# Kernel optimization log

Hardware: AMD Instinct MI355X
Metric: run time of the kernel (lower is better)

## Reference

```python
import math
import jax, jax.numpy as jnp
import numpy as np

LEVELS = 4          # wavelet_levels
PRUNE = 0.05        # wavelet_packet_prune_ratio
EPS = 1e-6
SQRT2 = math.sqrt(2.0)


def _haar_split(c):
    n = c.shape[-1]
    if n % 2 != 0:
        c = jnp.concatenate([c, jnp.zeros(c.shape[:-1] + (1,), c.dtype)], axis=-1)
    even, odd = c[..., 0::2], c[..., 1::2]
    return (even + odd) / SQRT2, (even - odd) / SQRT2, n


def _haar_merge(low, high, orig):
    even = (low + high) / SQRT2
    odd = (low - high) / SQRT2
    out = jnp.stack([even, odd], axis=-1).reshape(*low.shape[:-1], low.shape[-1] * 2)
    return out[..., :orig]


def _coherence(c, gpu):
    unit = c / jnp.maximum(jnp.abs(c), EPS)
    return jnp.clip(jnp.abs(jnp.mean(unit * jnp.conj(gpu), axis=-1, keepdims=True)), 0.0, 1.0)


def _cost(c, gpu):
    # gauge-aware packet cost: Shannon entropy of energy distribution + (1 - coherence)
    if c.shape[-1] <= 1:
        return jnp.float32(0.0)
    e = jnp.square(jnp.abs(c))
    p = jnp.maximum(e / jnp.maximum(e.sum(-1, keepdims=True), EPS), EPS)
    ent = -(p * jnp.log(p)).sum(-1)
    coh = _coherence(c, gpu)[..., 0]
    return jax.lax.stop_gradient(jnp.mean(ent + (1.0 - coh)))


def _band_center(path):
    if not path:
        return 0.0
    idx = 0
    for b in path:
        idx = (idx << 1) | b
    return (idx + 0.5) / (2 ** len(path))


def _leaf_gain(c, path, depth, gpu, Wp, bp, Wo, bo, lfg, sigma, hfg, cutoff):
    mag = jnp.maximum(jnp.abs(c), EPS)
    phase = jnp.arctan2(c.imag, c.real) / math.pi
    nle = jnp.broadcast_to(
        jnp.log(jnp.maximum(jnp.mean(jnp.square(jnp.abs(c)), -1, keepdims=True), EPS)), mag.shape)
    dn = jnp.full(mag.shape, depth / max(1, LEVELS), mag.dtype)
    bcv = _band_center(path)
    bc = jnp.full(mag.shape, bcv, mag.dtype)
    coh = jnp.broadcast_to(_coherence(c, gpu), mag.shape)
    pos = jnp.broadcast_to(jnp.linspace(0.0, 1.0, c.shape[-1], dtype=mag.dtype), mag.shape)
    feats = jnp.stack([jnp.log(mag), phase, nle, dn, bc, coh, pos], axis=-1)  # [..., n, 7]
    gd = jax.nn.silu(feats @ Wp.T + bp) @ Wo.T + bo                            # [..., n, 2]
    dm = 0.25 * jnp.tanh(gd[..., 0])
    dp = 0.5 * math.pi * jnp.tanh(gd[..., 1])
    lbb = 1.0 + lfg * jnp.exp(-(bcv * bcv) / jnp.square(sigma))
    hbd = hfg + (1.0 - hfg) * jax.nn.sigmoid((cutoff - bcv) / sigma)
    gm = lbb * hbd * (1.0 + lfg * coh) * (hfg + (1.0 - hfg) * coh) * jnp.exp(dm)
    return jax.lax.complex(gm * jnp.cos(dp), gm * jnp.sin(dp))  # torch.polar


def _filter_leaf(c, path, depth, total_e, gpu, params):
    Wp, bp, Wo, bo, lfg, sigma, hfg, cutoff = params
    node_e = jax.lax.stop_gradient(jnp.square(jnp.abs(c)).sum())
    filtered = c * _leaf_gain(c, path, depth, gpu, Wp, bp, Wo, bo, lfg, sigma, hfg, cutoff)
    coh_v = jax.lax.stop_gradient(jnp.mean(_coherence(c, gpu)))
    # spectral subtraction
    fm = jnp.abs(filtered)
    nf = jnp.median(fm, axis=-1, keepdims=True)
    damping = hfg + (1.0 - hfg) * jax.nn.sigmoid((cutoff - _band_center(path)) / sigma)
    den = jax.nn.relu(fm - (1.0 - damping) * nf)
    filtered = den * (filtered / jnp.maximum(fm, EPS))
    # prune low-energy / low-coherence leaves
    prune = jnp.logical_or(node_e / total_e < PRUNE, coh_v < PRUNE)
    return jnp.where(prune, filtered * jnp.square(hfg), filtered)


def _apply_node(c, depth, path, total_e, gpu, params):
    cost = _cost(c, gpu)
    leaf = _filter_leaf(c, path, depth, total_e, gpu, params)
    if depth >= LEVELS or c.shape[-1] <= 1:
        return leaf, cost
    low, high, orig = _haar_split(c)
    lr, lc = _apply_node(low, depth + 1, path + (0,), total_e, gpu, params)
    hr, hc = _apply_node(high, depth + 1, path + (1,), total_e, gpu, params)
    merged = _haar_merge(lr, hr, orig)
    child_cost = lc + hc
    # best-basis selection (wavelet_packet_best_basis=True)
    out = jnp.where(child_cost < cost, merged, leaf)
    return out, jnp.minimum(child_cost, cost)


def setup_inputs() -> dict:
    key = jax.random.key(0)
    ks = jax.random.split(key, 3)
    B, R, N = 8, 64, 8192
    x = jax.random.normal(ks[0], (B, R, N), jnp.float32)
    Wp = jax.random.normal(ks[1], (12, 7), jnp.float32) * math.sqrt(2.0 / 19.0)  # xavier-ish
    bp = jnp.zeros((12,), jnp.float32)
    Wo = jax.random.normal(ks[2], (2, 12), jnp.float32) * 0.1
    bo = jnp.zeros((2,), jnp.float32)
    return {"x": x, "Wp": Wp, "bp": bp, "Wo": Wo, "bo": bo,
            "lfg": jnp.float32(0.5), "sigma": jnp.float32(0.3),
            "hfg": jnp.float32(0.7), "cutoff": jnp.float32(0.25)}


def reference(x, Wp, bp, Wo, bo, lfg, sigma, hfg, cutoff):
    n = x.shape[-1]
    spec = jnp.fft.fft(x)  # complex64 [B, R, N]
    # _fft_filter spectral gating
    r2 = jnp.square(jnp.fft.fftfreq(n).astype(x.dtype))
    lfb = 1.0 + lfg * jnp.exp(-r2 / jnp.square(sigma))
    radius = jnp.sqrt(r2 + 1e-12)
    gate = jax.nn.sigmoid((cutoff - radius) / jnp.maximum(sigma, 0.05))
    spec = spec * (lfb * (hfg + (1.0 - hfg) * gate))
    # global phase unit
    unit = spec / jnp.maximum(jnp.abs(spec), EPS)
    g = jnp.mean(unit, axis=-1, keepdims=True)
    gpu = g / jnp.maximum(jnp.abs(g), EPS)
    total_e = jax.lax.stop_gradient(jnp.square(jnp.abs(spec)).sum())
    params = (Wp, bp, Wo, bo, lfg, sigma, hfg, cutoff)
    out, _ = _apply_node(spec, 0, (), total_e, gpu, params)
    return jnp.fft.ifft(out).real
```

## Files before the change

kernel.cpp:

```cpp
#include <hip/hip_runtime.h>
#include <hip/hip_fp16.h>
#include <math.h>

#define NN      8192
#define LOGN    13
#define ROWS    512
#define NT      512
#define NNODES  31
#define EPSF    1e-6f
#define PRUNEF  0.05f
#define SQRT1_2F 0.70710678118654752f
#define PIF      3.14159265358979323f
#define INV_PIF  0.31830988618379067f
#define HALF_PIF 1.57079632679489662f

typedef unsigned int uint;

__device__ __forceinline__ float fast_rcp(float x){ return __builtin_amdgcn_rcpf(x); }
__device__ __forceinline__ float fast_rsq(float x){ return __builtin_amdgcn_rsqf(x); }

__device__ __forceinline__ float tanh_pade(float y){
    y = fminf(3.f, fmaxf(-3.f, y));
    float y2 = y * y;
    float num = y * fmaf(y2, 10.f, 105.f);
    float den = fmaf(y2, 45.f, fmaf(y2 * y2, 1.f, 105.f));
    return num * fast_rcp(den);
}
__device__ __forceinline__ float silu_pade(float h){
    float y = fminf(3.f, fmaxf(-3.f, 0.5f * h));
    float y2 = y * y;
    float num = y * fmaf(y2, 10.f, 105.f);
    float den = fmaf(y2, 45.f, fmaf(y2 * y2, 1.f, 105.f));
    return 0.5f * h * (1.f + num * fast_rcp(den));
}
__device__ __forceinline__ float exp_small(float z){
    return fmaf(z, fmaf(z, fmaf(z, fmaf(z, 0.041666667f, 0.16666667f), 0.5f), 1.f), 1.f);
}
__device__ __forceinline__ float sin_halfpi(float t){
    float t2 = t * t;
    return t * fmaf(t2, fmaf(t2, fmaf(t2, -4.6817541e-3f, 7.96926262e-2f), -6.45964097e-1f), 1.57079632f);
}
__device__ __forceinline__ float cos_halfpi(float t){
    float t2 = t * t;
    return fmaf(t2, fmaf(t2, fmaf(t2, fmaf(t2, 9.1937e-4f, -2.08634807e-2f), 2.53669508e-1f), -1.23370055f), 1.f);
}

__device__ __forceinline__ float fast_atan2f(float y, float x) {
    float ay = fabsf(y), ax = fabsf(x);
    float mx = fmaxf(ax, ay), mn = fminf(ax, ay);
    float a = (mx > 0.f) ? (mn * fast_rcp(mx)) : 0.f;
    bool big = a > 0.4142135679f;
    float t = big ? ((a - 1.f) * fast_rcp(a + 1.f)) : a;
    float z2 = t * t;
    float p = fmaf(8.05374449538e-2f, z2, -1.38776856032e-1f);
    p = fmaf(p, z2, 1.99777106478e-1f);
    p = fmaf(p, z2, -3.33329491539e-1f);
    float r = fmaf(p * z2, t, t);
    if (big) r += 0.78539816339744831f;
    if (ay > ax) r = 1.57079632679489662f - r;
    if (x < 0.f) r = 3.14159265358979323f - r;
    return copysignf(r, y);
}

__device__ __forceinline__ float2 cmul(float2 a, float2 b){
    return make_float2(a.x*b.x - a.y*b.y, a.x*b.y + a.y*b.x);
}
__device__ __forceinline__ float2 cadd(float2 a, float2 b){ return make_float2(a.x+b.x, a.y+b.y); }
__device__ __forceinline__ float2 csub(float2 a, float2 b){ return make_float2(a.x-b.x, a.y-b.y); }

__device__ __forceinline__ uint pack_h2(float2 v){
    __half2 h = __floats2half2_rn(v.x, v.y);
    return __builtin_bit_cast(uint, h);
}
__device__ __forceinline__ float2 unpack_h2(uint u){
    __half2 h = __builtin_bit_cast(__half2, u);
    return make_float2(__low2float(h), __high2float(h));
}

__device__ __forceinline__ void wave_red8(float* a) {
    #pragma unroll
    for (int m = 32; m >= 1; m >>= 1) {
        #pragma unroll
        for (int q = 0; q < 8; ++q) a[q] += __shfl_xor(a[q], m);
    }
}

#define C8C 0.92387953251f
#define S8C 0.38268343236f
#define C4C 0.70710678119f

template<int HH, int LG>
__device__ __forceinline__ void fwd_r4_stage(float2* sh, int tid) {
    int j = tid & (HH - 1);
    float ang = (-PIF / (2.0f * (float)HH)) * (float)j;
    float s = __sinf(ang), co = __cosf(ang);
    float2 t1 = make_float2(co, s);
    float2 t2 = make_float2(co * co - s * s, 2.f * co * s);
    int g = tid & 127;
    int i = ((g >> LG) << (LG + 2)) | (g & (HH - 1));
    #pragma unroll
    for (int c = 0; c < 4; ++c) {
        int lb = (tid + (c << 9)) >> 7;
        int p = (lb << 9) + i;
        float2 a = sh[p], b = sh[p + HH], cc = sh[p + 2*HH], d = sh[p + 3*HH];
        float2 a1 = cadd(a, cc);
        float2 c1 = cmul(csub(a, cc), t1);
        float2 b1 = cadd(b, d);
        float2 u  = cmul(csub(b, d), t1);
        float2 d1 = make_float2(u.y, -u.x);
        sh[p]        = cadd(a1, b1);
        sh[p + HH]   = cmul(csub(a1, b1), t2);
        sh[p + 2*HH] = cadd(c1, d1);
        sh[p + 3*HH] = cmul(csub(c1, d1), t2);
    }
    __syncthreads();
}

template<int H, int LG>
__device__ __forceinline__ void inv_r4_stage(float2* sh, int tid) {
    int jj = tid & (H - 1);
    float ang = (PIF / (2.0f * (float)H)) * (float)jj;
    float s2 = __sinf(ang), c2 = __cosf(ang);
    float2 t2 = make_float2(c2, s2);
    float2 t1 = make_float2(c2 * c2 - s2 * s2, 2.f * c2 * s2);
    int g = tid & 127;
    int i = ((g >> LG) << (LG + 2)) | (g & (H - 1));
    #pragma unroll
    for (int c = 0; c < 4; ++c) {
        int lb = (tid + (c << 9)) >> 7;
        int p0 = (lb << 9) + i;
        float2 a = sh[p0], b = sh[p0 + H], cc = sh[p0 + 2*H], d = sh[p0 + 3*H];
        float2 tb = cmul(t1, b);
        float2 ap = cadd(a, tb), bp2 = csub(a, tb);
        float2 td = cmul(t1, d);
        float2 cp = cadd(cc, td), dp2 = csub(cc, td);
        float2 tc = cmul(t2, cp);
        float2 u  = cmul(t2, dp2);
        float2 iB = make_float2(-u.y, u.x);
        sh[p0]       = cadd(ap, tc);
        sh[p0 + H]   = cadd(bp2, iB);
        sh[p0 + 2*H] = csub(ap, tc);
        sh[p0 + 3*H] = csub(bp2, iB);
    }
    __syncthreads();
}

__global__ __launch_bounds__(NT, 4) void k_pre(
    const float* __restrict__ x, uint* __restrict__ Lv16,
    float* __restrict__ Se, float* __restrict__ Coh, float* __restrict__ Ent,
    const float* lfg_p, const float* sig_p, const float* hfg_p, const float* cut_p)
{
    __shared__ float2 sh[NN];
    __shared__ float4 wred[8];
    __shared__ float nacc[30 * 4];
    int row = blockIdx.x, tid = threadIdx.x;
    float lfg = *lfg_p, sigma = *sig_p, hfg = *hfg_p, cutoff = *cut_p;

    const float* xr = x + ((size_t)row << LOGN);
    float2 v[16];
    #pragma unroll
    for (int t = 0; t < 16; ++t)
        v[t] = make_float2(xr[tid + (t << 9)], 0.f);

    {
        float a0 = -PIF * (1.0f / 4096.0f) * (float)tid;
        float2 w1 = make_float2(__cosf(a0), __sinf(a0));
        float2 w2 = cmul(w1, w1);
        float2 w4 = cmul(w2, w2);
        float2 w8 = cmul(w4, w4);
        const float2 K16[8] = {
            { 1.f, 0.f}, { C8C, -S8C}, { C4C, -C4C}, { S8C, -C8C},
            { 0.f,-1.f}, {-S8C, -C8C}, {-C4C, -C4C}, {-C8C, -S8C}};
        #pragma unroll
        for (int t = 0; t < 8; ++t) {
            float2 W = cmul(w1, K16[t]);
            float2 a = v[t], b = v[t + 8];
            v[t] = cadd(a, b);
            v[t + 8] = cmul(csub(a, b), W);
        }
        const float2 K8a[4] = {{1.f,0.f},{C4C,-C4C},{0.f,-1.f},{-C4C,-C4C}};
        #pragma unroll
        for (int t = 0; t < 16; ++t) if (!(t & 4)) {
            float2 W = cmul(w2, K8a[t & 3]);
            float2 a = v[t], b = v[t + 4];
            v[t] = cadd(a, b);
            v[t + 4] = cmul(csub(a, b), W);
        }
        #pragma unroll
        for (int t = 0; t < 16; ++t) if (!(t & 2)) {
            float2 W = (t & 1) ? make_float2(w4.y, -w4.x) : w4;
            float2 a = v[t], b = v[t + 2];
            v[t] = cadd(a, b);
            v[t + 2] = cmul(csub(a, b), W);
        }
        #pragma unroll
        for (int t = 0; t < 16; ++t) if (!(t & 1)) {
            float2 a = v[t], b = v[t + 1];
            v[t] = cadd(a, b);
            v[t + 1] = cmul(csub(a, b), w8);
        }
    }

    if (tid < 120) nacc[tid] = 0.f;

    #pragma unroll
    for (int t = 0; t < 16; ++t) sh[tid + (t << 9)] = v[t];
    __syncthreads();
    fwd_r4_stage<128, 7>(sh, tid);
    fwd_r4_stage<32, 5>(sh, tid);
    fwd_r4_stage<8, 3>(sh, tid);
    fwd_r4_stage<2, 1>(sh, tid);
    #pragma unroll
    for (int c = 0; c < 8; ++c) {
        int p = (tid + (c << 9)) << 1;
        float2 a = sh[p], b = sh[p + 1];
        sh[p] = cadd(a, b);
        sh[p + 1] = csub(a, b);
    }
    __syncthreads();

    float inv_gs = 1.f / fmaxf(sigma, 0.05f);
    float is2 = 1.f / (sigma * sigma);
    float se = 0.f, slg = 0.f, sux = 0.f, suy = 0.f;
    #pragma unroll
    for (int t = 0; t < 16; ++t) {
        int p = tid + (t << 9);
        int k = (int)(__brev((uint)p) >> 19);
        float fk = (k < NN / 2) ? (float)k : (float)(k - NN);
        float f = fk * (1.0f / (float)NN);
        float r2 = f * f;
        float lfb = 1.f + lfg * __expf(-r2 * is2);
        float radius = sqrtf(r2 + 1e-12f);
        float gate = fast_rcp(1.f + __expf(-(cutoff - radius) * inv_gs));
        float mult = lfb * (hfg + (1.f - hfg) * gate);
        float2 c = sh[p];
        c.x *= mult; c.y *= mult;
        v[t] = c;
        float e = fmaf(c.x, c.x, c.y * c.y);
        se += e;
        slg += e * __logf(fmaxf(e, 1e-30f));
        float inv = fminf(fast_rsq(e), 1e6f);
        sux += c.x * inv; suy += c.y * inv;
    }
    #pragma unroll
    for (int m = 32; m >= 1; m >>= 1) {
        se += __shfl_xor(se, m); slg += __shfl_xor(slg, m);
        sux += __shfl_xor(sux, m); suy += __shfl_xor(suy, m);
    }
    if ((tid & 63) == 0) wred[tid >> 6] = make_float4(se, slg, sux, suy);
    __syncthreads();
    if (tid == 0) {
        float4 r = wred[0];
        #pragma unroll
        for (int w = 1; w < 8; ++w) {
            r.x += wred[w].x; r.y += wred[w].y; r.z += wred[w].z; r.w += wred[w].w;
        }
        float gx = r.z / (float)NN, gy = r.w / (float)NN;
        float ga = sqrtf(gx * gx + gy * gy);
        float denom = fmaxf(r.x, EPSF);
        Se[row]  = r.x;
        Ent[row] = __logf(denom) - r.y / denom;
        Coh[row] = fminf(ga, 1.f);
    }

    #pragma unroll
    for (int DP = 0; DP < 4; ++DP) {
        int ST = 8 >> DP;
        #pragma unroll
        for (int t = 0; t < 16; ++t) {
            if ((t & ST) == 0) {
                float2 a = v[t], b = v[t + ST];
                v[t]      = make_float2((a.x + b.x) * SQRT1_2F, (a.y + b.y) * SQRT1_2F);
                v[t + ST] = make_float2((a.x - b.x) * SQRT1_2F, (a.y - b.y) * SQRT1_2F);
            }
        }
        int CNT = 16 >> (DP + 1);
        int NPAIR = 1 << DP;
        int G0 = (2 << DP) - 1;
        #pragma unroll
        for (int pr = 0; pr < NPAIR; ++pr) {
            float acc[8] = {0,0,0,0,0,0,0,0};
            #pragma unroll
            for (int s = 0; s < 16; ++s) {
                int k0 = s - (2 * pr) * CNT;
                if (k0 >= 0 && k0 < CNT) {
                    float2 w = v[s];
                    float e = fmaf(w.x, w.x, w.y * w.y);
                    acc[0] += e; acc[1] += e * __logf(fmaxf(e, 1e-30f));
                    float iv = fminf(fast_rsq(e), 1e6f);
                    acc[2] += w.x * iv; acc[3] += w.y * iv;
                }
                int k1 = s - (2 * pr + 1) * CNT;
                if (k1 >= 0 && k1 < CNT) {
                    float2 w = v[s];
                    float e = fmaf(w.x, w.x, w.y * w.y);
                    acc[4] += e; acc[5] += e * __logf(fmaxf(e, 1e-30f));
                    float iv = fminf(fast_rsq(e), 1e6f);
                    acc[6] += w.x * iv; acc[7] += w.y * iv;
                }
            }
            wave_red8(acc);
            if ((tid & 63) == 0) {
                int ga = G0 + 2 * pr, gb = ga + 1;
                atomicAdd(&nacc[(ga-1)*4+0], acc[0]); atomicAdd(&nacc[(ga-1)*4+1], acc[1]);
                atomicAdd(&nacc[(ga-1)*4+2], acc[2]); atomicAdd(&nacc[(ga-1)*4+3], acc[3]);
                atomicAdd(&nacc[(gb-1)*4+0], acc[4]); atomicAdd(&nacc[(gb-1)*4+1], acc[5]);
                atomicAdd(&nacc[(gb-1)*4+2], acc[6]); atomicAdd(&nacc[(gb-1)*4+3], acc[7]);
            }
        }
    }
    __syncthreads();
    if (tid < 30) {
        int g = tid + 1;
        float E = nacc[tid * 4 + 0], SL = nacc[tid * 4 + 1];
        float ZX = nacc[tid * 4 + 2], ZY = nacc[tid * 4 + 3];
        float denom = fmaxf(E, EPSF);
        float ent = __logf(denom) - SL / denom;
        int d = 31 - __clz(g + 1);
        float invn = 1.f / (float)(NN >> d);
        float zx = ZX * invn, zy = ZY * invn;
        float ch = fminf(sqrtf(zx * zx + zy * zy), 1.f);
        Se[g * ROWS + row] = E; Coh[g * ROWS + row] = ch; Ent[g * ROWS + row] = ent;
    }

    uint* lrow = Lv16 + ((size_t)row << LOGN);
    #pragma unroll
    for (int t = 0; t < 16; ++t)
        lrow[tid + (t << 9)] = pack_h2(v[t]);
}

__global__ __launch_bounds__(NT) void k_decide(
    const float* __restrict__ Se, const float* __restrict__ Coh, const float* __restrict__ Ent,
    int* __restrict__ fFg, int* __restrict__ fPg)
{
    __shared__ float dtmp[3 * NNODES];
    __shared__ int fF[NNODES], fP[NNODES];
    int tid = threadIdx.x;
    float* dcost = dtmp; float* dne = dtmp + NNODES; float* dcm = dtmp + 2 * NNODES;
    int wid = tid >> 6, lane = tid & 63;
    for (int gn = wid; gn < NNODES; gn += 8) {
        float a = 0.f, b = 0.f, cc = 0.f;
        #pragma unroll
        for (int rr = 0; rr < ROWS / 64; ++rr) {
            int r = lane + (rr << 6);
            float ch = Coh[gn * ROWS + r];
            a += Ent[gn * ROWS + r] + 1.f - ch;
            b += Se[gn * ROWS + r];
            cc += ch;
        }
        #pragma unroll
        for (int m = 32; m >= 1; m >>= 1) {
            a += __shfl_xor(a, m); b += __shfl_xor(b, m); cc += __shfl_xor(cc, m);
        }
        if (lane == 0) { dcost[gn] = a / (float)ROWS; dne[gn] = b; dcm[gn] = cc / (float)ROWS; }
    }
    __syncthreads();
    if (tid == 0) {
        float mc[NNODES]; int sel[NNODES]; int act[NNODES];
        for (int gn = NNODES - 1; gn >= 0; --gn) {
            if (gn >= 15) { mc[gn] = dcost[gn]; sel[gn] = 0; }
            else {
                float chc = mc[2 * gn + 1] + mc[2 * gn + 2];
                sel[gn] = (chc < dcost[gn]) ? 1 : 0;
                mc[gn] = fminf(chc, dcost[gn]);
            }
        }
        float total_e = dne[0];
        act[0] = 1;
        for (int gn = 1; gn < NNODES; ++gn) {
            int p = (gn - 1) >> 1;
            act[gn] = act[p] && sel[p];
        }
        for (int gn = 0; gn < NNODES; ++gn) {
            int isleaf = (gn >= 15);
            fF[gn] = (act[gn] && (isleaf || !sel[gn])) ? 1 : 0;
            fP[gn] = ((dne[gn] / total_e < PRUNEF) || (dcm[gn] < PRUNEF)) ? 1 : 0;
        }
    }
    __syncthreads();
    if (tid < NNODES) { fFg[tid] = fF[tid]; fPg[tid] = fP[tid]; }
}

__device__ __forceinline__ uint key_of(float2 v) {
    return __float_as_uint(fmaf(v.x, v.x, v.y * v.y));
}
__device__ __forceinline__ uint key_at(const float2* sh, int p) { return key_of(sh[p]); }

__device__ __forceinline__ uint2 hist_locate1024(
    const uint* hist, int tid, uint r, uint* wsum, uint* selres)
{
    uint l0 = hist[2 * tid], l1 = hist[2 * tid + 1];
    uint s = l0 + l1;
    uint sc = s;
    #pragma unroll
    for (int o = 1; o < 64; o <<= 1) {
        uint v = __shfl_up(sc, o);
        if ((tid & 63) >= o) sc += v;
    }
    int wid = tid >> 6;
    if ((tid & 63) == 63) wsum[wid] = sc;
    __syncthreads();
    uint wb = 0;
    #pragma unroll
    for (int w = 0; w < 8; ++w) if (w < wid) wb += wsum[w];
    uint c0 = wb + sc - s;
    if (r >= c0 && r < c0 + l0) { selres[0] = 2u * tid;      selres[1] = c0; }
    c0 += l0;
    if (r >= c0 && r < c0 + l1) { selres[0] = 2u * tid + 1u; selres[1] = c0; }
    __syncthreads();
    uint2 res = make_uint2(selres[0], selres[1]);
    __syncthreads();
    return res;
}

template<int EPT>
__device__ __forceinline__ float median_node(
    const float2* sh, int nd, int tid,
    uint* hist, uint* wsum, uint* selres)
{
    uint r1 = (uint)(nd / 2 - 1), r2 = (uint)(nd / 2);
    for (int k = tid; k < 1024; k += NT) hist[k] = 0u;
    __syncthreads();
    #pragma unroll
    for (int c = 0; c < EPT; ++c)
        atomicAdd(&hist[key_at(sh, tid + (c << 9)) >> 21], 1u);
    __syncthreads();
    uint2 A1 = hist_locate1024(hist, tid, r1, wsum, selres);
    uint2 A2 = hist_locate1024(hist, tid, r2, wsum, selres);
    uint va, vb;
    if (A1.x != A2.x) {
        if (tid == 0) { selres[0] = 0u; selres[1] = 0xFFFFFFFFu; }
        __syncthreads();
        #pragma unroll
        for (int c = 0; c < EPT; ++c) {
            uint k = key_at(sh, tid + (c << 9));
            uint b = k >> 21;
            if (b == A1.x) atomicMax(&selres[0], k);
            if (b == A2.x) atomicMin(&selres[1], k);
        }
        __syncthreads();
        va = selres[0]; vb = selres[1];
        __syncthreads();
    } else {
        uint p1 = A1.x;
        for (int k = tid; k < 1024; k += NT) hist[k] = 0u;
        __syncthreads();
        #pragma unroll
        for (int c = 0; c < EPT; ++c) {
            uint k = key_at(sh, tid + (c << 9));
            if ((k >> 21) == p1) atomicAdd(&hist[(k >> 11) & 1023u], 1u);
        }
        __syncthreads();
        uint2 B1 = hist_locate1024(hist, tid, r1 - A1.y, wsum, selres);
        uint2 B2 = hist_locate1024(hist, tid, r2 - A1.y, wsum, selres);
        if (B1.x != B2.x) {
            uint pA = (p1 << 10) | B1.x, pB = (p1 << 10) | B2.x;
            if (tid == 0) { selres[0] = 0u; selres[1] = 0xFFFFFFFFu; }
            __syncthreads();
            #pragma unroll
            for (int c = 0; c < EPT; ++c) {
                uint k = key_at(sh, tid + (c << 9));
                uint b = k >> 11;
                if (b == pA) atomicMax(&selres[0], k);
                if (b == pB) atomicMin(&selres[1], k);
            }
            __syncthreads();
            va = selres[0]; vb = selres[1];
            __syncthreads();
        } else {
            uint pfx = (p1 << 10) | B1.x;
            for (int k = tid; k < 1024; k += NT) hist[k] = 0u;
            __syncthreads();
            #pragma unroll
            for (int c = 0; c < EPT; ++c) {
                uint k = key_at(sh, tid + (c << 9));
                if ((k >> 11) == pfx) atomicAdd(&hist[(k >> 1) & 1023u], 1u);
            }
            __syncthreads();
            uint2 C1 = hist_locate1024(hist, tid, r1 - A1.y - B1.y, wsum, selres);
            uint2 C2 = hist_locate1024(hist, tid, r2 - A1.y - B1.y, wsum, selres);
            va = ((pfx << 10) | C1.x) << 1;
            vb = ((pfx << 10) | C2.x) << 1;
        }
    }
    return 0.5f * (sqrtf(__uint_as_float(va)) + sqrtf(__uint_as_float(vb)));
}

__device__ __forceinline__ float median_root_reg(
    const float2 (&v)[16], int tid, uint* hist, uint* wsum, uint* selres)
{
    const uint r1 = NN / 2 - 1, r2 = NN / 2;
    for (int k = tid; k < 1024; k += NT) hist[k] = 0u;
    __syncthreads();
    #pragma unroll
    for (int t = 0; t < 16; ++t)
        atomicAdd(&hist[key_of(v[t]) >> 21], 1u);
    __syncthreads();
    uint2 A1 = hist_locate1024(hist, tid, r1, wsum, selres);
    uint2 A2 = hist_locate1024(hist, tid, r2, wsum, selres);
    uint va, vb;
    if (A1.x != A2.x) {
        if (tid == 0) { selres[0] = 0u; selres[1] = 0xFFFFFFFFu; }
        __syncthreads();
        #pragma unroll
        for (int t = 0; t < 16; ++t) {
            uint k = key_of(v[t]);
            uint b = k >> 21;
            if (b == A1.x) atomicMax(&selres[0], k);
            if (b == A2.x) atomicMin(&selres[1], k);
        }
        __syncthreads();
        va = selres[0]; vb = selres[1];
        __syncthreads();
    } else {
        uint p1 = A1.x;
        for (int k = tid; k < 1024; k += NT) hist[k] = 0u;
        __syncthreads();
        #pragma unroll
        for (int t = 0; t < 16; ++t) {
            uint k = key_of(v[t]);
            if ((k >> 21) == p1) atomicAdd(&hist[(k >> 11) & 1023u], 1u);
        }
        __syncthreads();
        uint2 B1 = hist_locate1024(hist, tid, r1 - A1.y, wsum, selres);
        uint2 B2 = hist_locate1024(hist, tid, r2 - A1.y, wsum, selres);
        if (B1.x != B2.x) {
            uint pA = (p1 << 10) | B1.x, pB = (p1 << 10) | B2.x;
            if (tid == 0) { selres[0] = 0u; selres[1] = 0xFFFFFFFFu; }
            __syncthreads();
            #pragma unroll
            for (int t = 0; t < 16; ++t) {
                uint k = key_of(v[t]);
                uint b = k >> 11;
                if (b == pA) atomicMax(&selres[0], k);
                if (b == pB) atomicMin(&selres[1], k);
            }
            __syncthreads();
            va = selres[0]; vb = selres[1];
            __syncthreads();
        } else {
            uint pfx = (p1 << 10) | B1.x;
            for (int k = tid; k < 1024; k += NT) hist[k] = 0u;
            __syncthreads();
            #pragma unroll
            for (int t = 0; t < 16; ++t) {
                uint k = key_of(v[t]);
                if ((k >> 11) == pfx) atomicAdd(&hist[(k >> 1) & 1023u], 1u);
            }
            __syncthreads();
            uint2 C1 = hist_locate1024(hist, tid, r1 - A1.y - B1.y, wsum, selres);
            uint2 C2 = hist_locate1024(hist, tid, r2 - A1.y - B1.y, wsum, selres);
            va = ((pfx << 10) | C1.x) << 1;
            vb = ((pfx << 10) | C2.x) << 1;
        }
    }
    return 0.5f * (sqrtf(__uint_as_float(va)) + sqrtf(__uint_as_float(vb)));
}

struct NodeConst {
    float hbd, gbase, hb[12], bo0, bo1;
};
__device__ __forceinline__ NodeConst node_consts(
    int D, int nodes, int n, int g, int ND, int row,
    const float* __restrict__ Wp, const float* __restrict__ bp,
    const float* __restrict__ Wo, const float* __restrict__ bo,
    const float* __restrict__ Se, const float* __restrict__ Coh,
    float lfg, float sigma, float hfg, float cutoff)
{
    NodeConst nc;
    float bcv = (D == 0) ? 0.f : ((float)n + 0.5f) / (float)nodes;
    float coh = Coh[g * ROWS + row];
    float sev = Se[g * ROWS + row];
    float nle = __logf(fmaxf(sev * (1.f / (float)ND), EPSF));
    float dnv = (float)D * 0.25f;
    float lbb = 1.f + lfg * __expf(-(bcv * bcv) / (sigma * sigma));
    nc.hbd = hfg + (1.f - hfg) * fast_rcp(1.f + __expf(-(cutoff - bcv) / sigma));
    nc.gbase = lbb * nc.hbd * (1.f + lfg * coh) * (hfg + (1.f - hfg) * coh);
    #pragma unroll
    for (int j = 0; j < 12; ++j)
        nc.hb[j] = bp[j] + nle * Wp[j*7+2] + dnv * Wp[j*7+3] + bcv * Wp[j*7+4] + coh * Wp[j*7+5];
    nc.bo0 = bo[0]; nc.bo1 = bo[1];
    return nc;
}

__device__ __forceinline__ float2 mlp_apply(
    float2 cv, int o, int D, float invnm1, const NodeConst& nc,
    const float* __restrict__ Wp, const float* __restrict__ Wo)
{
    float m2 = fmaf(cv.x, cv.x, cv.y * cv.y);
    float f0 = 0.5f * __logf(fmaxf(m2, 1e-12f));
    float f1 = fast_atan2f(cv.y, cv.x) * INV_PIF;
    int itrue = (int)(__brev((uint)o) >> (19 + D));
    float f6 = (float)itrue * invnm1;
    float acc0 = nc.bo0, acc1 = nc.bo1;
    #pragma unroll
    for (int j = 0; j < 12; ++j) {
        float h = fmaf(f0, Wp[j*7], fmaf(f1, Wp[j*7+1], fmaf(f6, Wp[j*7+6], nc.hb[j])));
        float s = silu_pade(h);
        acc0 = fmaf(s, Wo[j], acc0);
        acc1 = fmaf(s, Wo[12 + j], acc1);
    }
    float gm = nc.gbase * exp_small(0.25f * tanh_pade(acc0));
    float tp = tanh_pade(acc1);
    float spv = sin_halfpi(tp), cpv = cos_halfpi(tp);
    return make_float2(gm * (cv.x * cpv - cv.y * spv),
                       gm * (cv.x * spv + cv.y * cpv));
}

template<int D>
__device__ __forceinline__ void filter_node_sh(
    float2 (&v)[16], int n, int tid, float2* sh,
    const float* __restrict__ Wp, const float* __restrict__ bp,
    const float* __restrict__ Wo, const float* __restrict__ bo,
    const float* __restrict__ Se, const float* __restrict__ Coh,
    const int* __restrict__ fPg, int row,
    uint* hist, uint* wsum, uint* selres,
    float lfg, float sigma, float hfg, float cutoff)
{
    constexpr int CNT = 16 >> D;
    constexpr int ND  = NN >> D;
    constexpr int EPT = ND >> 9;
    int g = (1 << D) - 1 + n;

    #pragma unroll
    for (int t = 0; t < 16; ++t) {
        int k = t - n * CNT;
        if ((unsigned)k < (unsigned)CNT) sh[tid + (k << 9)] = v[t];
    }
    __syncthreads();

    NodeConst nc = node_consts(D, 1 << D, n, g, ND, row, Wp, bp, Wo, bo, Se, Coh,
                               lfg, sigma, hfg, cutoff);
    float invnm1 = 1.f / (float)(ND - 1);

    #pragma unroll
    for (int c = 0; c < EPT; ++c) {
        int o = tid + (c << 9);
        sh[o] = mlp_apply(sh[o], o, D, invnm1, nc, Wp, Wo);
    }
    __syncthreads();

    float nf = median_node<EPT>(sh, ND, tid, hist, wsum, selres);
    float thr = (1.f - nc.hbd) * nf;
    float pf = fPg[g] ? (hfg * hfg) : 1.f;

    #pragma unroll
    for (int c = 0; c < EPT; ++c) {
        int o = tid + (c << 9);
        float2 w = sh[o];
        float fm = sqrtf(fmaf(w.x, w.x, w.y * w.y));
        float den = fmaxf(fm - thr, 0.f);
        float s = den * fast_rcp(fmaxf(fm, EPSF)) * pf;
        sh[o] = make_float2(w.x * s, w.y * s);
    }
    __syncthreads();

    #pragma unroll
    for (int t = 0; t < 16; ++t) {
        int k = t - n * CNT;
        if ((unsigned)k < (unsigned)CNT) v[t] = sh[tid + (k << 9)];
    }
    __syncthreads();
}

__device__ __forceinline__ void filter_root_reg(
    float2 (&v)[16], int tid,
    const float* __restrict__ Wp, const float* __restrict__ bp,
    const float* __restrict__ Wo, const float* __restrict__ bo,
    const float* __restrict__ Se, const float* __restrict__ Coh,
    const int* __restrict__ fPg, int row,
    uint* hist, uint* wsum, uint* selres,
    float lfg, float sigma, float hfg, float cutoff)
{
    NodeConst nc = node_consts(0, 1, 0, 0, NN, row, Wp, bp, Wo, bo, Se, Coh,
                               lfg, sigma, hfg, cutoff);
    float invnm1 = 1.f / (float)(NN - 1);

    #pragma unroll
    for (int t = 0; t < 16; ++t) {
        int o = tid + (t << 9);
        v[t] = mlp_apply(v[t], o, 0, invnm1, nc, Wp, Wo);
    }

    float nf = median_root_reg(v, tid, hist, wsum, selres);
    float thr = (1.f - nc.hbd) * nf;
    float pf = fPg[0] ? (hfg * hfg) : 1.f;

    #pragma unroll
    for (int t = 0; t < 16; ++t) {
        float2 w = v[t];
        float fm = sqrtf(fmaf(w.x, w.x, w.y * w.y));
        float den = fmaxf(fm - thr, 0.f);
        float s = den * fast_rcp(fmaxf(fm, EPSF)) * pf;
        v[t] = make_float2(w.x * s, w.y * s);
    }
}

template<int DT>
__device__ __forceinline__ void merge_reg(float2 (&v)[16]){
    #pragma unroll
    for (int t = 0; t < 16; ++t) {
        if ((t & DT) == 0) {
            float2 lo = v[t], hi = v[t + DT];
            v[t]      = make_float2((lo.x + hi.x) * SQRT1_2F, (lo.y + hi.y) * SQRT1_2F);
            v[t + DT] = make_float2((lo.x - hi.x) * SQRT1_2F, (lo.y - hi.y) * SQRT1_2F);
        }
    }
}

__global__ __launch_bounds__(NT, 4) void k_rest(
    const uint* __restrict__ Lv16,
    const float* __restrict__ Se, const float* __restrict__ Coh,
    const int* __restrict__ fFg, const int* __restrict__ fPg,
    float* __restrict__ out,
    const float* __restrict__ Wp, const float* __restrict__ bp,
    const float* __restrict__ Wo, const float* __restrict__ bo,
    const float* lfg_p, const float* sig_p, const float* hfg_p, const float* cut_p)
{
    __shared__ float2 sh[NN];
    __shared__ __align__(16) uint hist[1024];
    __shared__ uint wsum[8];
    __shared__ uint selres[2];

    int row = blockIdx.x, tid = threadIdx.x;
    float lfg = *lfg_p, sigma = *sig_p, hfg = *hfg_p, cutoff = *cut_p;

    const uint* lr = Lv16 + ((size_t)row << LOGN);
    uint raw[16];
    #pragma unroll
    for (int t = 0; t < 16; ++t) raw[t] = lr[tid + (t << 9)];

    float2 v[16];
    #pragma unroll
    for (int t = 0; t < 16; ++t) v[t] = unpack_h2(raw[t]);

    for (int n = 0; n < 16; ++n)
        if (fFg[15 + n])
            filter_node_sh<4>(v, n, tid, sh, Wp, bp, Wo, bo, Se, Coh, fPg, row, hist, wsum, selres, lfg, sigma, hfg, cutoff);
    merge_reg<1>(v);
    for (int n = 0; n < 8; ++n)
        if (fFg[7 + n])
            filter_node_sh<3>(v, n, tid, sh, Wp, bp, Wo, bo, Se, Coh, fPg, row, hist, wsum, selres, lfg, sigma, hfg, cutoff);
    merge_reg<2>(v);
    for (int n = 0; n < 4; ++n)
        if (fFg[3 + n])
            filter_node_sh<2>(v, n, tid, sh, Wp, bp, Wo, bo, Se, Coh, fPg, row, hist, wsum, selres, lfg, sigma, hfg, cutoff);
    merge_reg<4>(v);
    for (int n = 0; n < 2; ++n)
        if (fFg[1 + n])
            filter_node_sh<1>(v, n, tid, sh, Wp, bp, Wo, bo, Se, Coh, fPg, row, hist, wsum, selres, lfg, sigma, hfg, cutoff);
    merge_reg<8>(v);
    if (fFg[0])
        filter_root_reg(v, tid, Wp, bp, Wo, bo, Se, Coh, fPg, row, hist, wsum, selres, lfg, sigma, hfg, cutoff);

    #pragma unroll
    for (int t = 0; t < 16; ++t) sh[tid + (t << 9)] = v[t];
    __syncthreads();

    inv_r4_stage<1, 0>(sh, tid);
    inv_r4_stage<4, 2>(sh, tid);
    inv_r4_stage<16, 4>(sh, tid);
    inv_r4_stage<64, 6>(sh, tid);
    {
        int jj = tid & 255;
        float ang = (PIF / 256.0f) * (float)jj;
        float2 W = make_float2(__cosf(ang), __sinf(ang));
        #pragma unroll
        for (int c = 0; c < 8; ++c) {
            int q = tid + (c << 9);
            int lb = q >> 8;
            int p = (lb << 9) + jj;
            float2 a = sh[p], b = sh[p + 256];
            float2 tb = cmul(W, b);
            sh[p] = cadd(a, tb);
            sh[p + 256] = csub(a, tb);
        }
        __syncthreads();
    }

    #pragma unroll
    for (int t = 0; t < 16; ++t) v[t] = sh[tid + (t << 9)];
    {
        float a0 = PIF * (1.0f / 4096.0f) * (float)tid;
        float2 w1 = make_float2(__cosf(a0), __sinf(a0));
        float2 w2 = cmul(w1, w1);
        float2 w4 = cmul(w2, w2);
        float2 w8 = cmul(w4, w4);
        #pragma unroll
        for (int t = 0; t < 16; ++t) if (!(t & 1)) {
            float2 tb = cmul(w8, v[t + 1]);
            float2 a = v[t];
            v[t] = cadd(a, tb);
            v[t + 1] = csub(a, tb);
        }
        #pragma unroll
        for (int t = 0; t < 16; ++t) if (!(t & 2)) {
            float2 W = (t & 1) ? make_float2(-w4.y, w4.x) : w4;
            float2 tb = cmul(W, v[t + 2]);
            float2 a = v[t];
            v[t] = cadd(a, tb);
            v[t + 2] = csub(a, tb);
        }
        const float2 K8p[4] = {{1.f,0.f},{C4C,C4C},{0.f,1.f},{-C4C,C4C}};
        #pragma unroll
        for (int t = 0; t < 16; ++t) if (!(t & 4)) {
            float2 W = cmul(w2, K8p[t & 3]);
            float2 tb = cmul(W, v[t + 4]);
            float2 a = v[t];
            v[t] = cadd(a, tb);
            v[t + 4] = csub(a, tb);
        }
        const float2 K16p[8] = {
            { 1.f, 0.f}, { C8C, S8C}, { C4C, C4C}, { S8C, C8C},
            { 0.f, 1.f}, {-S8C, C8C}, {-C4C, C4C}, {-C8C, S8C}};
        #pragma unroll
        for (int t = 0; t < 8; ++t) {
            float2 W = cmul(w1, K16p[t]);
            float2 tb = cmul(W, v[t + 8]);
            float2 a = v[t];
            v[t] = cadd(a, tb);
            v[t + 8] = csub(a, tb);
        }
    }

    float* orow = out + ((size_t)row << LOGN);
    #pragma unroll
    for (int t = 0; t < 16; ++t)
        orow[tid + (t << 9)] = v[t].x * (1.0f / (float)NN);
}

extern "C" void kernel_launch(void* const* d_in, const int* in_sizes, int n_in,
                              void* d_out, int out_size, void* d_ws, size_t ws_size,
                              hipStream_t stream) {
    const float* x   = (const float*)d_in[0];
    const float* Wp  = (const float*)d_in[1];
    const float* bp  = (const float*)d_in[2];
    const float* Wo  = (const float*)d_in[3];
    const float* bo  = (const float*)d_in[4];
    const float* lfg = (const float*)d_in[5];
    const float* sig = (const float*)d_in[6];
    const float* hfg = (const float*)d_in[7];
    const float* cut = (const float*)d_in[8];
    float* out = (float*)d_out;

    size_t LVB = (size_t)ROWS * NN * sizeof(uint);
    char* ws = (char*)d_ws;
    uint*   Lv16 = (uint*)ws;
    float*  Se   = (float*)(ws + LVB);
    float*  Coh  = Se  + (size_t)NNODES * ROWS;
    float*  Ent  = Coh + (size_t)NNODES * ROWS;
    int*    fFg  = (int*)(Ent + (size_t)NNODES * ROWS);
    int*    fPg  = fFg + NNODES;
    size_t need = (size_t)((char*)(fPg + NNODES) - ws);
    if (ws_size < need) return;

    dim3 b(NT);
    k_pre   <<<dim3(ROWS), b, 0, stream>>>(x, Lv16, Se, Coh, Ent, lfg, sig, hfg, cut);
    k_decide<<<dim3(1),    b, 0, stream>>>(Se, Coh, Ent, fFg, fPg);
    k_rest  <<<dim3(ROWS), b, 0, stream>>>(Lv16, Se, Coh, fFg, fPg, out, Wp, bp, Wo, bo, lfg, sig, hfg, cut);
}
```

Baseline: 131.3 us.

## Double threads per row to 1024 and restructure FFT and wavelet stages for 8 elements per thread

Raises the block size from 512 to 1024 threads, so each thread holds 8 complex values instead of 16. The in-register radix-16 FFT prologue and epilogue become radix-8, and the shared-memory radix-4 stages are re-indexed. The last wavelet split and merge level now goes through shared memory, and the per-node median and filter code is made generic over node size. The intent is more wave-level parallelism and lower register pressure per thread, at the cost of extra shared-memory round-trips, more __syncthreads barriers and more atomics per block.

```diff
diff --git a/kernel.cpp b/kernel.cpp
--- a/kernel.cpp
+++ b/kernel.cpp
@@ -5,14 +5,13 @@
 #define NN      8192
 #define LOGN    13
 #define ROWS    512
-#define NT      512
+#define NT      1024
 #define NNODES  31
 #define EPSF    1e-6f
 #define PRUNEF  0.05f
 #define SQRT1_2F 0.70710678118654752f
 #define PIF      3.14159265358979323f
 #define INV_PIF  0.31830988618379067f
-#define HALF_PIF 1.57079632679489662f
 
 typedef unsigned int uint;
 
@@ -85,8 +84,6 @@
     }
 }
 
-#define C8C 0.92387953251f
-#define S8C 0.38268343236f
 #define C4C 0.70710678119f
 
 template<int HH, int LG>
@@ -96,12 +93,10 @@
     float s = __sinf(ang), co = __cosf(ang);
     float2 t1 = make_float2(co, s);
     float2 t2 = make_float2(co * co - s * s, 2.f * co * s);
-    int g = tid & 127;
-    int i = ((g >> LG) << (LG + 2)) | (g & (HH - 1));
-    #pragma unroll
-    for (int c = 0; c < 4; ++c) {
-        int lb = (tid + (c << 9)) >> 7;
-        int p = (lb << 9) + i;
+    #pragma unroll
+    for (int c = 0; c < 2; ++c) {
+        int q = tid + (c << 10);
+        int p = ((q >> LG) << (LG + 2)) | j;
         float2 a = sh[p], b = sh[p + HH], cc = sh[p + 2*HH], d = sh[p + 3*HH];
         float2 a1 = cadd(a, cc);
         float2 c1 = cmul(csub(a, cc), t1);
@@ -123,12 +118,10 @@
     float s2 = __sinf(ang), c2 = __cosf(ang);
     float2 t2 = make_float2(c2, s2);
     float2 t1 = make_float2(c2 * c2 - s2 * s2, 2.f * c2 * s2);
-    int g = tid & 127;
-    int i = ((g >> LG) << (LG + 2)) | (g & (H - 1));
-    #pragma unroll
-    for (int c = 0; c < 4; ++c) {
-        int lb = (tid + (c << 9)) >> 7;
-        int p0 = (lb << 9) + i;
+    #pragma unroll
+    for (int c = 0; c < 2; ++c) {
+        int q = tid + (c << 10);
+        int p0 = ((q >> LG) << (LG + 2)) | jj;
         float2 a = sh[p0], b = sh[p0 + H], cc = sh[p0 + 2*H], d = sh[p0 + 3*H];
         float2 tb = cmul(t1, b);
         float2 ap = cadd(a, tb), bp2 = csub(a, tb);
@@ -145,86 +138,82 @@
     __syncthreads();
 }
 
-__global__ __launch_bounds__(NT, 4) void k_pre(
+__global__ __launch_bounds__(NT, 8) void k_pre(
     const float* __restrict__ x, uint* __restrict__ Lv16,
     float* __restrict__ Se, float* __restrict__ Coh, float* __restrict__ Ent,
     const float* lfg_p, const float* sig_p, const float* hfg_p, const float* cut_p)
 {
     __shared__ float2 sh[NN];
-    __shared__ float4 wred[8];
+    __shared__ float4 wred[16];
     __shared__ float nacc[30 * 4];
     int row = blockIdx.x, tid = threadIdx.x;
     float lfg = *lfg_p, sigma = *sig_p, hfg = *hfg_p, cutoff = *cut_p;
 
     const float* xr = x + ((size_t)row << LOGN);
-    float2 v[16];
-    #pragma unroll
-    for (int t = 0; t < 16; ++t)
-        v[t] = make_float2(xr[tid + (t << 9)], 0.f);
+    float2 v[8];
+    #pragma unroll
+    for (int t = 0; t < 8; ++t)
+        v[t] = make_float2(xr[tid + (t << 10)], 0.f);
 
     {
         float a0 = -PIF * (1.0f / 4096.0f) * (float)tid;
         float2 w1 = make_float2(__cosf(a0), __sinf(a0));
         float2 w2 = cmul(w1, w1);
         float2 w4 = cmul(w2, w2);
-        float2 w8 = cmul(w4, w4);
-        const float2 K16[8] = {
-            { 1.f, 0.f}, { C8C, -S8C}, { C4C, -C4C}, { S8C, -C8C},
-            { 0.f,-1.f}, {-S8C, -C8C}, {-C4C, -C4C}, {-C8C, -S8C}};
-        #pragma unroll
-        for (int t = 0; t < 8; ++t) {
-            float2 W = cmul(w1, K16[t]);
-            float2 a = v[t], b = v[t + 8];
-            v[t] = cadd(a, b);
-            v[t + 8] = cmul(csub(a, b), W);
-        }
-        const float2 K8a[4] = {{1.f,0.f},{C4C,-C4C},{0.f,-1.f},{-C4C,-C4C}};
-        #pragma unroll
-        for (int t = 0; t < 16; ++t) if (!(t & 4)) {
-            float2 W = cmul(w2, K8a[t & 3]);
+        const float2 K4m[4] = {{1.f,0.f},{C4C,-C4C},{0.f,-1.f},{-C4C,-C4C}};
+        #pragma unroll
+        for (int t = 0; t < 4; ++t) {
+            float2 W = cmul(w1, K4m[t]);
             float2 a = v[t], b = v[t + 4];
             v[t] = cadd(a, b);
             v[t + 4] = cmul(csub(a, b), W);
         }
         #pragma unroll
-        for (int t = 0; t < 16; ++t) if (!(t & 2)) {
-            float2 W = (t & 1) ? make_float2(w4.y, -w4.x) : w4;
+        for (int t = 0; t < 8; ++t) if (!(t & 2)) {
+            float2 W = (t & 1) ? make_float2(w2.y, -w2.x) : w2;
             float2 a = v[t], b = v[t + 2];
             v[t] = cadd(a, b);
             v[t + 2] = cmul(csub(a, b), W);
         }
         #pragma unroll
-        for (int t = 0; t < 16; ++t) if (!(t & 1)) {
+        for (int t = 0; t < 8; ++t) if (!(t & 1)) {
             float2 a = v[t], b = v[t + 1];
             v[t] = cadd(a, b);
-            v[t + 1] = cmul(csub(a, b), w8);
-        }
+            v[t + 1] = cmul(csub(a, b), w4);
+        }
+    }
+
+    #pragma unroll
+    for (int t = 0; t < 8; ++t) sh[tid + (t << 10)] = v[t];
+    __syncthreads();
+    fwd_r4_stage<256, 8>(sh, tid);
+    fwd_r4_stage<64, 6>(sh, tid);
+    fwd_r4_stage<16, 4>(sh, tid);
+    fwd_r4_stage<4, 2>(sh, tid);
+    {
+        #pragma unroll
+        for (int c = 0; c < 2; ++c) {
+            int p = (tid + (c << 10)) << 2;
+            float2 a = sh[p], b = sh[p+1], cc = sh[p+2], d = sh[p+3];
+            float2 a1 = cadd(a, cc), c1 = csub(a, cc);
+            float2 b1 = cadd(b, d);
+            float2 u  = csub(b, d);
+            float2 d1 = make_float2(u.y, -u.x);
+            sh[p]   = cadd(a1, b1);
+            sh[p+1] = csub(a1, b1);
+            sh[p+2] = cadd(c1, d1);
+            sh[p+3] = csub(c1, d1);
+        }
+        __syncthreads();
     }
 
     if (tid < 120) nacc[tid] = 0.f;
-
-    #pragma unroll
-    for (int t = 0; t < 16; ++t) sh[tid + (t << 9)] = v[t];
-    __syncthreads();
-    fwd_r4_stage<128, 7>(sh, tid);
-    fwd_r4_stage<32, 5>(sh, tid);
-    fwd_r4_stage<8, 3>(sh, tid);
-    fwd_r4_stage<2, 1>(sh, tid);
-    #pragma unroll
-    for (int c = 0; c < 8; ++c) {
-        int p = (tid + (c << 9)) << 1;
-        float2 a = sh[p], b = sh[p + 1];
-        sh[p] = cadd(a, b);
-        sh[p + 1] = csub(a, b);
-    }
-    __syncthreads();
-
     float inv_gs = 1.f / fmaxf(sigma, 0.05f);
     float is2 = 1.f / (sigma * sigma);
     float se = 0.f, slg = 0.f, sux = 0.f, suy = 0.f;
     #pragma unroll
-    for (int t = 0; t < 16; ++t) {
-        int p = tid + (t << 9);
+    for (int t = 0; t < 8; ++t) {
+        int p = tid + (t << 10);
         int k = (int)(__brev((uint)p) >> 19);
         float fk = (k < NN / 2) ? (float)k : (float)(k - NN);
         float f = fk * (1.0f / (float)NN);
@@ -252,7 +241,7 @@
     if (tid == 0) {
         float4 r = wred[0];
         #pragma unroll
-        for (int w = 1; w < 8; ++w) {
+        for (int w = 1; w < 16; ++w) {
             r.x += wred[w].x; r.y += wred[w].y; r.z += wred[w].z; r.w += wred[w].w;
         }
         float gx = r.z / (float)NN, gy = r.w / (float)NN;
@@ -263,50 +252,129 @@
         Coh[row] = fminf(ga, 1.f);
     }
 
-    #pragma unroll
-    for (int DP = 0; DP < 4; ++DP) {
-        int ST = 8 >> DP;
-        #pragma unroll
-        for (int t = 0; t < 16; ++t) {
-            if ((t & ST) == 0) {
-                float2 a = v[t], b = v[t + ST];
-                v[t]      = make_float2((a.x + b.x) * SQRT1_2F, (a.y + b.y) * SQRT1_2F);
-                v[t + ST] = make_float2((a.x - b.x) * SQRT1_2F, (a.y - b.y) * SQRT1_2F);
-            }
-        }
-        int CNT = 16 >> (DP + 1);
-        int NPAIR = 1 << DP;
-        int G0 = (2 << DP) - 1;
-        #pragma unroll
-        for (int pr = 0; pr < NPAIR; ++pr) {
+    {
+        #pragma unroll
+        for (int t = 0; t < 4; ++t) {
+            float2 a = v[t], b = v[t + 4];
+            v[t]     = make_float2((a.x + b.x) * SQRT1_2F, (a.y + b.y) * SQRT1_2F);
+            v[t + 4] = make_float2((a.x - b.x) * SQRT1_2F, (a.y - b.y) * SQRT1_2F);
+        }
+        float acc[8] = {0,0,0,0,0,0,0,0};
+        #pragma unroll
+        for (int s = 0; s < 4; ++s) {
+            float2 w = v[s];
+            float e = fmaf(w.x, w.x, w.y * w.y);
+            acc[0] += e; acc[1] += e * __logf(fmaxf(e, 1e-30f));
+            float iv = fminf(fast_rsq(e), 1e6f);
+            acc[2] += w.x * iv; acc[3] += w.y * iv;
+            float2 h = v[s + 4];
+            float e2 = fmaf(h.x, h.x, h.y * h.y);
+            acc[4] += e2; acc[5] += e2 * __logf(fmaxf(e2, 1e-30f));
+            float iv2 = fminf(fast_rsq(e2), 1e6f);
+            acc[6] += h.x * iv2; acc[7] += h.y * iv2;
+        }
+        wave_red8(acc);
+        if ((tid & 63) == 0) {
+            atomicAdd(&nacc[0], acc[0]); atomicAdd(&nacc[1], acc[1]);
+            atomicAdd(&nacc[2], acc[2]); atomicAdd(&nacc[3], acc[3]);
+            atomicAdd(&nacc[4], acc[4]); atomicAdd(&nacc[5], acc[5]);
+            atomicAdd(&nacc[6], acc[6]); atomicAdd(&nacc[7], acc[7]);
+        }
+    }
+    {
+        #pragma unroll
+        for (int t = 0; t < 8; ++t) if (!(t & 2)) {
+            float2 a = v[t], b = v[t + 2];
+            v[t]     = make_float2((a.x + b.x) * SQRT1_2F, (a.y + b.y) * SQRT1_2F);
+            v[t + 2] = make_float2((a.x - b.x) * SQRT1_2F, (a.y - b.y) * SQRT1_2F);
+        }
+        #pragma unroll
+        for (int pr = 0; pr < 2; ++pr) {
             float acc[8] = {0,0,0,0,0,0,0,0};
             #pragma unroll
-            for (int s = 0; s < 16; ++s) {
-                int k0 = s - (2 * pr) * CNT;
-                if (k0 >= 0 && k0 < CNT) {
-                    float2 w = v[s];
-                    float e = fmaf(w.x, w.x, w.y * w.y);
-                    acc[0] += e; acc[1] += e * __logf(fmaxf(e, 1e-30f));
-                    float iv = fminf(fast_rsq(e), 1e6f);
-                    acc[2] += w.x * iv; acc[3] += w.y * iv;
-                }
-                int k1 = s - (2 * pr + 1) * CNT;
-                if (k1 >= 0 && k1 < CNT) {
-                    float2 w = v[s];
-                    float e = fmaf(w.x, w.x, w.y * w.y);
-                    acc[4] += e; acc[5] += e * __logf(fmaxf(e, 1e-30f));
-                    float iv = fminf(fast_rsq(e), 1e6f);
-                    acc[6] += w.x * iv; acc[7] += w.y * iv;
-                }
+            for (int s = 0; s < 2; ++s) {
+                float2 w = v[4 * pr + s];
+                float e = fmaf(w.x, w.x, w.y * w.y);
+                acc[0] += e; acc[1] += e * __logf(fmaxf(e, 1e-30f));
+                float iv = fminf(fast_rsq(e), 1e6f);
+                acc[2] += w.x * iv; acc[3] += w.y * iv;
+                float2 h = v[4 * pr + 2 + s];
+                float e2 = fmaf(h.x, h.x, h.y * h.y);
+                acc[4] += e2; acc[5] += e2 * __logf(fmaxf(e2, 1e-30f));
+                float iv2 = fminf(fast_rsq(e2), 1e6f);
+                acc[6] += h.x * iv2; acc[7] += h.y * iv2;
             }
             wave_red8(acc);
             if ((tid & 63) == 0) {
-                int ga = G0 + 2 * pr, gb = ga + 1;
+                int ga = 3 + 2 * pr, gb = ga + 1;
                 atomicAdd(&nacc[(ga-1)*4+0], acc[0]); atomicAdd(&nacc[(ga-1)*4+1], acc[1]);
                 atomicAdd(&nacc[(ga-1)*4+2], acc[2]); atomicAdd(&nacc[(ga-1)*4+3], acc[3]);
                 atomicAdd(&nacc[(gb-1)*4+0], acc[4]); atomicAdd(&nacc[(gb-1)*4+1], acc[5]);
                 atomicAdd(&nacc[(gb-1)*4+2], acc[6]); atomicAdd(&nacc[(gb-1)*4+3], acc[7]);
             }
+        }
+    }
+    {
+        #pragma unroll
+        for (int t = 0; t < 8; ++t) if (!(t & 1)) {
+            float2 a = v[t], b = v[t + 1];
+            v[t]     = make_float2((a.x + b.x) * SQRT1_2F, (a.y + b.y) * SQRT1_2F);
+            v[t + 1] = make_float2((a.x - b.x) * SQRT1_2F, (a.y - b.y) * SQRT1_2F);
+        }
+        #pragma unroll
+        for (int pr = 0; pr < 4; ++pr) {
+            float acc[8] = {0,0,0,0,0,0,0,0};
+            {
+                float2 w = v[2 * pr];
+                float e = fmaf(w.x, w.x, w.y * w.y);
+                acc[0] = e; acc[1] = e * __logf(fmaxf(e, 1e-30f));
+                float iv = fminf(fast_rsq(e), 1e6f);
+                acc[2] = w.x * iv; acc[3] = w.y * iv;
+                float2 h = v[2 * pr + 1];
+                float e2 = fmaf(h.x, h.x, h.y * h.y);
+                acc[4] = e2; acc[5] = e2 * __logf(fmaxf(e2, 1e-30f));
+                float iv2 = fminf(fast_rsq(e2), 1e6f);
+                acc[6] = h.x * iv2; acc[7] = h.y * iv2;
+            }
+            wave_red8(acc);
+            if ((tid & 63) == 0) {
+                int ga = 7 + 2 * pr, gb = ga + 1;
+                atomicAdd(&nacc[(ga-1)*4+0], acc[0]); atomicAdd(&nacc[(ga-1)*4+1], acc[1]);
+                atomicAdd(&nacc[(ga-1)*4+2], acc[2]); atomicAdd(&nacc[(ga-1)*4+3], acc[3]);
+                atomicAdd(&nacc[(gb-1)*4+0], acc[4]); atomicAdd(&nacc[(gb-1)*4+1], acc[5]);
+                atomicAdd(&nacc[(gb-1)*4+2], acc[6]); atomicAdd(&nacc[(gb-1)*4+3], acc[7]);
+            }
+        }
+    }
+
+    #pragma unroll
+    for (int t = 0; t < 8; ++t) sh[tid + (t << 10)] = v[t];
+    __syncthreads();
+    #pragma unroll
+    for (int t = 0; t < 4; ++t) {
+        int q = tid + (t << 10);
+        int p = ((q >> 9) << 10) | (q & 511);
+        float2 a = sh[p], b = sh[p + 512];
+        float2 lo = make_float2((a.x + b.x) * SQRT1_2F, (a.y + b.y) * SQRT1_2F);
+        float2 hi = make_float2((a.x - b.x) * SQRT1_2F, (a.y - b.y) * SQRT1_2F);
+        sh[p] = lo; sh[p + 512] = hi;
+        float acc[8];
+        float e = fmaf(lo.x, lo.x, lo.y * lo.y);
+        acc[0] = e; acc[1] = e * __logf(fmaxf(e, 1e-30f));
+        float iv = fminf(fast_rsq(e), 1e6f);
+        acc[2] = lo.x * iv; acc[3] = lo.y * iv;
+        float e2 = fmaf(hi.x, hi.x, hi.y * hi.y);
+        acc[4] = e2; acc[5] = e2 * __logf(fmaxf(e2, 1e-30f));
+        float iv2 = fminf(fast_rsq(e2), 1e6f);
+        acc[6] = hi.x * iv2; acc[7] = hi.y * iv2;
+        wave_red8(acc);
+        if ((tid & 63) == 0) {
+            int ca = (q >> 9) << 1;
+            int ia = (14 + ca) * 4;
+            atomicAdd(&nacc[ia+0], acc[0]); atomicAdd(&nacc[ia+1], acc[1]);
+            atomicAdd(&nacc[ia+2], acc[2]); atomicAdd(&nacc[ia+3], acc[3]);
+            atomicAdd(&nacc[ia+4], acc[4]); atomicAdd(&nacc[ia+5], acc[5]);
+            atomicAdd(&nacc[ia+6], acc[6]); atomicAdd(&nacc[ia+7], acc[7]);
         }
     }
     __syncthreads();
@@ -325,11 +393,13 @@
 
     uint* lrow = Lv16 + ((size_t)row << LOGN);
     #pragma unroll
-    for (int t = 0; t < 16; ++t)
-        lrow[tid + (t << 9)] = pack_h2(v[t]);
-}
-
-__global__ __launch_bounds__(NT) void k_decide(
+    for (int t = 0; t < 8; ++t) {
+        int k = tid + (t << 10);
+        lrow[k] = pack_h2(sh[k]);
+    }
+}
+
+__global__ __launch_bounds__(512) void k_decide(
     const float* __restrict__ Se, const float* __restrict__ Coh, const float* __restrict__ Ent,
     int* __restrict__ fFg, int* __restrict__ fPg)
 {
@@ -384,56 +454,47 @@
 __device__ __forceinline__ uint key_of(float2 v) {
     return __float_as_uint(fmaf(v.x, v.x, v.y * v.y));
 }
-__device__ __forceinline__ uint key_at(const float2* sh, int p) { return key_of(sh[p]); }
-
-__device__ __forceinline__ uint2 hist_locate1024(
+
+__device__ __forceinline__ uint2 hist_locate1k(
     const uint* hist, int tid, uint r, uint* wsum, uint* selres)
 {
-    uint l0 = hist[2 * tid], l1 = hist[2 * tid + 1];
-    uint s = l0 + l1;
+    uint s = hist[tid];
     uint sc = s;
     #pragma unroll
     for (int o = 1; o < 64; o <<= 1) {
-        uint v = __shfl_up(sc, o);
-        if ((tid & 63) >= o) sc += v;
+        uint u = __shfl_up(sc, o);
+        if ((tid & 63) >= o) sc += u;
     }
     int wid = tid >> 6;
     if ((tid & 63) == 63) wsum[wid] = sc;
     __syncthreads();
     uint wb = 0;
     #pragma unroll
-    for (int w = 0; w < 8; ++w) if (w < wid) wb += wsum[w];
+    for (int w = 0; w < 16; ++w) if (w < wid) wb += wsum[w];
     uint c0 = wb + sc - s;
-    if (r >= c0 && r < c0 + l0) { selres[0] = 2u * tid;      selres[1] = c0; }
-    c0 += l0;
-    if (r >= c0 && r < c0 + l1) { selres[0] = 2u * tid + 1u; selres[1] = c0; }
+    if (r >= c0 && r < c0 + s) { selres[0] = (uint)tid; selres[1] = c0; }
     __syncthreads();
     uint2 res = make_uint2(selres[0], selres[1]);
     __syncthreads();
     return res;
 }
 
-template<int EPT>
-__device__ __forceinline__ float median_node(
-    const float2* sh, int nd, int tid,
-    uint* hist, uint* wsum, uint* selres)
+__device__ float median_dyn(
+    const float2* sh, int nd, int tid, uint* hist, uint* wsum, uint* selres)
 {
     uint r1 = (uint)(nd / 2 - 1), r2 = (uint)(nd / 2);
-    for (int k = tid; k < 1024; k += NT) hist[k] = 0u;
-    __syncthreads();
-    #pragma unroll
-    for (int c = 0; c < EPT; ++c)
-        atomicAdd(&hist[key_at(sh, tid + (c << 9)) >> 21], 1u);
-    __syncthreads();
-    uint2 A1 = hist_locate1024(hist, tid, r1, wsum, selres);
-    uint2 A2 = hist_locate1024(hist, tid, r2, wsum, selres);
+    if (tid < 1024) hist[tid] = 0u;
+    __syncthreads();
+    for (int i = tid; i < nd; i += NT) atomicAdd(&hist[key_of(sh[i]) >> 21], 1u);
+    __syncthreads();
+    uint2 A1 = hist_locate1k(hist, tid, r1, wsum, selres);
+    uint2 A2 = hist_locate1k(hist, tid, r2, wsum, selres);
     uint va, vb;
     if (A1.x != A2.x) {
         if (tid == 0) { selres[0] = 0u; selres[1] = 0xFFFFFFFFu; }
         __syncthreads();
-        #pragma unroll
-        for (int c = 0; c < EPT; ++c) {
-            uint k = key_at(sh, tid + (c << 9));
+        for (int i = tid; i < nd; i += NT) {
+            uint k = key_of(sh[i]);
             uint b = k >> 21;
             if (b == A1.x) atomicMax(&selres[0], k);
             if (b == A2.x) atomicMin(&selres[1], k);
@@ -443,23 +504,21 @@
         __syncthreads();
     } else {
         uint p1 = A1.x;
-        for (int k = tid; k < 1024; k += NT) hist[k] = 0u;
-        __syncthreads();
-        #pragma unroll
-        for (int c = 0; c < EPT; ++c) {
-            uint k = key_at(sh, tid + (c << 9));
+        if (tid < 1024) hist[tid] = 0u;
+        __syncthreads();
+        for (int i = tid; i < nd; i += NT) {
+            uint k = key_of(sh[i]);
             if ((k >> 21) == p1) atomicAdd(&hist[(k >> 11) & 1023u], 1u);
         }
         __syncthreads();
-        uint2 B1 = hist_locate1024(hist, tid, r1 - A1.y, wsum, selres);
-        uint2 B2 = hist_locate1024(hist, tid, r2 - A1.y, wsum, selres);
+        uint2 B1 = hist_locate1k(hist, tid, r1 - A1.y, wsum, selres);
+        uint2 B2 = hist_locate1k(hist, tid, r2 - A1.y, wsum, selres);
         if (B1.x != B2.x) {
             uint pA = (p1 << 10) | B1.x, pB = (p1 << 10) | B2.x;
             if (tid == 0) { selres[0] = 0u; selres[1] = 0xFFFFFFFFu; }
             __syncthreads();
-            #pragma unroll
-            for (int c = 0; c < EPT; ++c) {
-                uint k = key_at(sh, tid + (c << 9));
+            for (int i = tid; i < nd; i += NT) {
+                uint k = key_of(sh[i]);
                 uint b = k >> 11;
                 if (b == pA) atomicMax(&selres[0], k);
                 if (b == pB) atomicMin(&selres[1], k);
@@ -469,16 +528,15 @@
             __syncthreads();
         } else {
             uint pfx = (p1 << 10) | B1.x;
-            for (int k = tid; k < 1024; k += NT) hist[k] = 0u;
+            if (tid < 1024) hist[tid] = 0u;
             __syncthreads();
-            #pragma unroll
-            for (int c = 0; c < EPT; ++c) {
-                uint k = key_at(sh, tid + (c << 9));
+            for (int i = tid; i < nd; i += NT) {
+                uint k = key_of(sh[i]);
                 if ((k >> 11) == pfx) atomicAdd(&hist[(k >> 1) & 1023u], 1u);
             }
             __syncthreads();
-            uint2 C1 = hist_locate1024(hist, tid, r1 - A1.y - B1.y, wsum, selres);
-            uint2 C2 = hist_locate1024(hist, tid, r2 - A1.y - B1.y, wsum, selres);
+            uint2 C1 = hist_locate1k(hist, tid, r1 - A1.y - B1.y, wsum, selres);
+            uint2 C2 = hist_locate1k(hist, tid, r2 - A1.y - B1.y, wsum, selres);
             va = ((pfx << 10) | C1.x) << 1;
             vb = ((pfx << 10) | C2.x) << 1;
         }
@@ -487,23 +545,22 @@
 }
 
 __device__ __forceinline__ float median_root_reg(
-    const float2 (&v)[16], int tid, uint* hist, uint* wsum, uint* selres)
+    const float2 (&v)[8], int tid, uint* hist, uint* wsum, uint* selres)
 {
     const uint r1 = NN / 2 - 1, r2 = NN / 2;
-    for (int k = tid; k < 1024; k += NT) hist[k] = 0u;
-    __syncthreads();
-    #pragma unroll
-    for (int t = 0; t < 16; ++t)
-        atomicAdd(&hist[key_of(v[t]) >> 21], 1u);
-    __syncthreads();
-    uint2 A1 = hist_locate1024(hist, tid, r1, wsum, selres);
-    uint2 A2 = hist_locate1024(hist, tid, r2, wsum, selres);
+    hist[tid] = 0u;
+    __syncthreads();
+    #pragma unroll
+    for (int t = 0; t < 8; ++t) atomicAdd(&hist[key_of(v[t]) >> 21], 1u);
+    __syncthreads();
+    uint2 A1 = hist_locate1k(hist, tid, r1, wsum, selres);
+    uint2 A2 = hist_locate1k(hist, tid, r2, wsum, selres);
     uint va, vb;
     if (A1.x != A2.x) {
         if (tid == 0) { selres[0] = 0u; selres[1] = 0xFFFFFFFFu; }
         __syncthreads();
         #pragma unroll
-        for (int t = 0; t < 16; ++t) {
+        for (int t = 0; t < 8; ++t) {
             uint k = key_of(v[t]);
             uint b = k >> 21;
             if (b == A1.x) atomicMax(&selres[0], k);
@@ -514,22 +571,22 @@
         __syncthreads();
     } else {
         uint p1 = A1.x;
-        for (int k = tid; k < 1024; k += NT) hist[k] = 0u;
-        __syncthreads();
-        #pragma unroll
-        for (int t = 0; t < 16; ++t) {
+        hist[tid] = 0u;
+        __syncthreads();
+        #pragma unroll
+        for (int t = 0; t < 8; ++t) {
             uint k = key_of(v[t]);
             if ((k >> 21) == p1) atomicAdd(&hist[(k >> 11) & 1023u], 1u);
         }
         __syncthreads();
-        uint2 B1 = hist_locate1024(hist, tid, r1 - A1.y, wsum, selres);
-        uint2 B2 = hist_locate1024(hist, tid, r2 - A1.y, wsum, selres);
+        uint2 B1 = hist_locate1k(hist, tid, r1 - A1.y, wsum, selres);
+        uint2 B2 = hist_locate1k(hist, tid, r2 - A1.y, wsum, selres);
         if (B1.x != B2.x) {
             uint pA = (p1 << 10) | B1.x, pB = (p1 << 10) | B2.x;
             if (tid == 0) { selres[0] = 0u; selres[1] = 0xFFFFFFFFu; }
             __syncthreads();
             #pragma unroll
-            for (int t = 0; t < 16; ++t) {
+            for (int t = 0; t < 8; ++t) {
                 uint k = key_of(v[t]);
                 uint b = k >> 11;
                 if (b == pA) atomicMax(&selres[0], k);
@@ -540,16 +597,16 @@
             __syncthreads();
         } else {
             uint pfx = (p1 << 10) | B1.x;
-            for (int k = tid; k < 1024; k += NT) hist[k] = 0u;
+            hist[tid] = 0u;
             __syncthreads();
             #pragma unroll
-            for (int t = 0; t < 16; ++t) {
+            for (int t = 0; t < 8; ++t) {
                 uint k = key_of(v[t]);
                 if ((k >> 11) == pfx) atomicAdd(&hist[(k >> 1) & 1023u], 1u);
             }
             __syncthreads();
-            uint2 C1 = hist_locate1024(hist, tid, r1 - A1.y - B1.y, wsum, selres);
-            uint2 C2 = hist_locate1024(hist, tid, r2 - A1.y - B1.y, wsum, selres);
+            uint2 C1 = hist_locate1k(hist, tid, r1 - A1.y - B1.y, wsum, selres);
+            uint2 C2 = hist_locate1k(hist, tid, r2 - A1.y - B1.y, wsum, selres);
             va = ((pfx << 10) | C1.x) << 1;
             vb = ((pfx << 10) | C2.x) << 1;
         }
@@ -607,9 +664,8 @@
                        gm * (cv.x * spv + cv.y * cpv));
 }
 
-template<int D>
-__device__ __forceinline__ void filter_node_sh(
-    float2 (&v)[16], int n, int tid, float2* sh,
+__device__ __forceinline__ void filter_generic(
+    int D, int n, float2 (&v)[8], int tid, float2* sh,
     const float* __restrict__ Wp, const float* __restrict__ bp,
     const float* __restrict__ Wo, const float* __restrict__ bo,
     const float* __restrict__ Se, const float* __restrict__ Coh,
@@ -617,54 +673,59 @@
     uint* hist, uint* wsum, uint* selres,
     float lfg, float sigma, float hfg, float cutoff)
 {
-    constexpr int CNT = 16 >> D;
-    constexpr int ND  = NN >> D;
-    constexpr int EPT = ND >> 9;
+    int nd = NN >> D;
     int g = (1 << D) - 1 + n;
-
-    #pragma unroll
-    for (int t = 0; t < 16; ++t) {
-        int k = t - n * CNT;
-        if ((unsigned)k < (unsigned)CNT) sh[tid + (k << 9)] = v[t];
-    }
-    __syncthreads();
-
-    NodeConst nc = node_consts(D, 1 << D, n, g, ND, row, Wp, bp, Wo, bo, Se, Coh,
+    if (D <= 3) {
+        int CNT = 8 >> D;
+        #pragma unroll
+        for (int t = 0; t < 8; ++t) {
+            int k = t - n * CNT;
+            if ((unsigned)k < (unsigned)CNT) sh[tid + (k << 10)] = v[t];
+        }
+    } else {
+        bool own = ((tid >> 9) == (n & 1));
+        #pragma unroll
+        for (int t = 0; t < 8; ++t)
+            if (t == (n >> 1) && own) sh[tid & 511] = v[t];
+    }
+    __syncthreads();
+
+    NodeConst nc = node_consts(D, 1 << D, n, g, nd, row, Wp, bp, Wo, bo, Se, Coh,
                                lfg, sigma, hfg, cutoff);
-    float invnm1 = 1.f / (float)(ND - 1);
-
-    #pragma unroll
-    for (int c = 0; c < EPT; ++c) {
-        int o = tid + (c << 9);
-        sh[o] = mlp_apply(sh[o], o, D, invnm1, nc, Wp, Wo);
-    }
-    __syncthreads();
-
-    float nf = median_node<EPT>(sh, ND, tid, hist, wsum, selres);
+    float invnm1 = 1.f / (float)(nd - 1);
+    for (int i = tid; i < nd; i += NT)
+        sh[i] = mlp_apply(sh[i], i, D, invnm1, nc, Wp, Wo);
+    __syncthreads();
+
+    float nf = median_dyn(sh, nd, tid, hist, wsum, selres);
     float thr = (1.f - nc.hbd) * nf;
     float pf = fPg[g] ? (hfg * hfg) : 1.f;
-
-    #pragma unroll
-    for (int c = 0; c < EPT; ++c) {
-        int o = tid + (c << 9);
-        float2 w = sh[o];
+    for (int i = tid; i < nd; i += NT) {
+        float2 w = sh[i];
         float fm = sqrtf(fmaf(w.x, w.x, w.y * w.y));
         float den = fmaxf(fm - thr, 0.f);
         float s = den * fast_rcp(fmaxf(fm, EPSF)) * pf;
-        sh[o] = make_float2(w.x * s, w.y * s);
-    }
-    __syncthreads();
-
-    #pragma unroll
-    for (int t = 0; t < 16; ++t) {
-        int k = t - n * CNT;
-        if ((unsigned)k < (unsigned)CNT) v[t] = sh[tid + (k << 9)];
+        sh[i] = make_float2(w.x * s, w.y * s);
+    }
+    __syncthreads();
+    if (D <= 3) {
+        int CNT = 8 >> D;
+        #pragma unroll
+        for (int t = 0; t < 8; ++t) {
+            int k = t - n * CNT;
+            if ((unsigned)k < (unsigned)CNT) v[t] = sh[tid + (k << 10)];
+        }
+    } else {
+        bool own = ((tid >> 9) == (n & 1));
+        #pragma unroll
+        for (int t = 0; t < 8; ++t)
+            if (t == (n >> 1) && own) v[t] = sh[tid & 511];
     }
     __syncthreads();
 }
 
 __device__ __forceinline__ void filter_root_reg(
-    float2 (&v)[16], int tid,
+    float2 (&v)[8], int tid,
     const float* __restrict__ Wp, const float* __restrict__ bp,
     const float* __restrict__ Wo, const float* __restrict__ bo,
     const float* __restrict__ Se, const float* __restrict__ Coh,
@@ -675,19 +736,16 @@
     NodeConst nc = node_consts(0, 1, 0, 0, NN, row, Wp, bp, Wo, bo, Se, Coh,
                                lfg, sigma, hfg, cutoff);
     float invnm1 = 1.f / (float)(NN - 1);
-
-    #pragma unroll
-    for (int t = 0; t < 16; ++t) {
-        int o = tid + (t << 9);
+    #pragma unroll
+    for (int t = 0; t < 8; ++t) {
+        int o = tid + (t << 10);
         v[t] = mlp_apply(v[t], o, 0, invnm1, nc, Wp, Wo);
     }
-
     float nf = median_root_reg(v, tid, hist, wsum, selres);
     float thr = (1.f - nc.hbd) * nf;
     float pf = fPg[0] ? (hfg * hfg) : 1.f;
-
-    #pragma unroll
-    for (int t = 0; t < 16; ++t) {
+    #pragma unroll
+    for (int t = 0; t < 8; ++t) {
         float2 w = v[t];
         float fm = sqrtf(fmaf(w.x, w.x, w.y * w.y));
         float den = fmaxf(fm - thr, 0.f);
@@ -697,9 +755,9 @@
 }
 
 template<int DT>
-__device__ __forceinline__ void merge_reg(float2 (&v)[16]){
-    #pragma unroll
-    for (int t = 0; t < 16; ++t) {
+__device__ __forceinline__ void merge_reg(float2 (&v)[8]){
+    #pragma unroll
+    for (int t = 0; t < 8; ++t) {
         if ((t & DT) == 0) {
             float2 lo = v[t], hi = v[t + DT];
             v[t]      = make_float2((lo.x + hi.x) * SQRT1_2F, (lo.y + hi.y) * SQRT1_2F);
@@ -708,7 +766,7 @@
     }
 }
 
-__global__ __launch_bounds__(NT, 4) void k_rest(
+__global__ __launch_bounds__(NT, 8) void k_rest(
     const uint* __restrict__ Lv16,
     const float* __restrict__ Se, const float* __restrict__ Coh,
     const int* __restrict__ fFg, const int* __restrict__ fPg,
@@ -719,114 +777,96 @@
 {
     __shared__ float2 sh[NN];
     __shared__ __align__(16) uint hist[1024];
-    __shared__ uint wsum[8];
+    __shared__ uint wsum[16];
     __shared__ uint selres[2];
 
     int row = blockIdx.x, tid = threadIdx.x;
     float lfg = *lfg_p, sigma = *sig_p, hfg = *hfg_p, cutoff = *cut_p;
 
     const uint* lr = Lv16 + ((size_t)row << LOGN);
-    uint raw[16];
-    #pragma unroll
-    for (int t = 0; t < 16; ++t) raw[t] = lr[tid + (t << 9)];
-
-    float2 v[16];
-    #pragma unroll
-    for (int t = 0; t < 16; ++t) v[t] = unpack_h2(raw[t]);
+    float2 v[8];
+    #pragma unroll
+    for (int t = 0; t < 8; ++t) v[t] = unpack_h2(lr[tid + (t << 10)]);
 
     for (int n = 0; n < 16; ++n)
         if (fFg[15 + n])
-            filter_node_sh<4>(v, n, tid, sh, Wp, bp, Wo, bo, Se, Coh, fPg, row, hist, wsum, selres, lfg, sigma, hfg, cutoff);
-    merge_reg<1>(v);
+            filter_generic(4, n, v, tid, sh, Wp, bp, Wo, bo, Se, Coh, fPg, row, hist, wsum, selres, lfg, sigma, hfg, cutoff);
+
+    #pragma unroll
+    for (int t = 0; t < 8; ++t) sh[tid + (t << 10)] = v[t];
+    __syncthreads();
+    #pragma unroll
+    for (int t = 0; t < 4; ++t) {
+        int q = tid + (t << 10);
+        int p = ((q >> 9) << 10) | (q & 511);
+        float2 a = sh[p], b = sh[p + 512];
+        sh[p]       = make_float2((a.x + b.x) * SQRT1_2F, (a.y + b.y) * SQRT1_2F);
+        sh[p + 512] = make_float2((a.x - b.x) * SQRT1_2F, (a.y - b.y) * SQRT1_2F);
+    }
+    __syncthreads();
+    #pragma unroll
+    for (int t = 0; t < 8; ++t) v[t] = sh[tid + (t << 10)];
+    __syncthreads();
+
     for (int n = 0; n < 8; ++n)
         if (fFg[7 + n])
-            filter_node_sh<3>(v, n, tid, sh, Wp, bp, Wo, bo, Se, Coh, fPg, row, hist, wsum, selres, lfg, sigma, hfg, cutoff);
-    merge_reg<2>(v);
+            filter_generic(3, n, v, tid, sh, Wp, bp, Wo, bo, Se, Coh, fPg, row, hist, wsum, selres, lfg, sigma, hfg, cutoff);
+    merge_reg<1>(v);
     for (int n = 0; n < 4; ++n)
         if (fFg[3 + n])
-            filter_node_sh<2>(v, n, tid, sh, Wp, bp, Wo, bo, Se, Coh, fPg, row, hist, wsum, selres, lfg, sigma, hfg, cutoff);
-    merge_reg<4>(v);
+            filter_generic(2, n, v, tid, sh, Wp, bp, Wo, bo, Se, Coh, fPg, row, hist, wsum, selres, lfg, sigma, hfg, cutoff);
+    merge_reg<2>(v);
     for (int n = 0; n < 2; ++n)
         if (fFg[1 + n])
-            filter_node_sh<1>(v, n, tid, sh, Wp, bp, Wo, bo, Se, Coh, fPg, row, hist, wsum, selres, lfg, sigma, hfg, cutoff);
-    merge_reg<8>(v);
+            filter_generic(1, n, v, tid, sh, Wp, bp, Wo, bo, Se, Coh, fPg, row, hist, wsum, selres, lfg, sigma, hfg, cutoff);
+    merge_reg<4>(v);
     if (fFg[0])
         filter_root_reg(v, tid, Wp, bp, Wo, bo, Se, Coh, fPg, row, hist, wsum, selres, lfg, sigma, hfg, cutoff);
 
     #pragma unroll
-    for (int t = 0; t < 16; ++t) sh[tid + (t << 9)] = v[t];
-    __syncthreads();
-
+    for (int t = 0; t < 8; ++t) sh[tid + (t << 10)] = v[t];
+    __syncthreads();
     inv_r4_stage<1, 0>(sh, tid);
     inv_r4_stage<4, 2>(sh, tid);
     inv_r4_stage<16, 4>(sh, tid);
     inv_r4_stage<64, 6>(sh, tid);
-    {
-        int jj = tid & 255;
-        float ang = (PIF / 256.0f) * (float)jj;
-        float2 W = make_float2(__cosf(ang), __sinf(ang));
-        #pragma unroll
-        for (int c = 0; c < 8; ++c) {
-            int q = tid + (c << 9);
-            int lb = q >> 8;
-            int p = (lb << 9) + jj;
-            float2 a = sh[p], b = sh[p + 256];
-            float2 tb = cmul(W, b);
-            sh[p] = cadd(a, tb);
-            sh[p + 256] = csub(a, tb);
-        }
-        __syncthreads();
-    }
-
-    #pragma unroll
-    for (int t = 0; t < 16; ++t) v[t] = sh[tid + (t << 9)];
+    inv_r4_stage<256, 8>(sh, tid);
+    #pragma unroll
+    for (int t = 0; t < 8; ++t) v[t] = sh[tid + (t << 10)];
     {
         float a0 = PIF * (1.0f / 4096.0f) * (float)tid;
         float2 w1 = make_float2(__cosf(a0), __sinf(a0));
         float2 w2 = cmul(w1, w1);
         float2 w4 = cmul(w2, w2);
-        float2 w8 = cmul(w4, w4);
-        #pragma unroll
-        for (int t = 0; t < 16; ++t) if (!(t & 1)) {
-            float2 tb = cmul(w8, v[t + 1]);
+        #pragma unroll
+        for (int t = 0; t < 8; ++t) if (!(t & 1)) {
+            float2 tb = cmul(w4, v[t + 1]);
             float2 a = v[t];
             v[t] = cadd(a, tb);
             v[t + 1] = csub(a, tb);
         }
         #pragma unroll
-        for (int t = 0; t < 16; ++t) if (!(t & 2)) {
-            float2 W = (t & 1) ? make_float2(-w4.y, w4.x) : w4;
+        for (int t = 0; t < 8; ++t) if (!(t & 2)) {
+            float2 W = (t & 1) ? make_float2(-w2.y, w2.x) : w2;
             float2 tb = cmul(W, v[t + 2]);
             float2 a = v[t];
             v[t] = cadd(a, tb);
             v[t + 2] = csub(a, tb);
         }
-        const float2 K8p[4] = {{1.f,0.f},{C4C,C4C},{0.f,1.f},{-C4C,C4C}};
-        #pragma unroll
-        for (int t = 0; t < 16; ++t) if (!(t & 4)) {
-            float2 W = cmul(w2, K8p[t & 3]);
+        const float2 K4p[4] = {{1.f,0.f},{C4C,C4C},{0.f,1.f},{-C4C,C4C}};
+        #pragma unroll
+        for (int t = 0; t < 4; ++t) {
+            float2 W = cmul(w1, K4p[t]);
             float2 tb = cmul(W, v[t + 4]);
             float2 a = v[t];
             v[t] = cadd(a, tb);
             v[t + 4] = csub(a, tb);
         }
-        const float2 K16p[8] = {
-            { 1.f, 0.f}, { C8C, S8C}, { C4C, C4C}, { S8C, C8C},
-            { 0.f, 1.f}, {-S8C, C8C}, {-C4C, C4C}, {-C8C, S8C}};
-        #pragma unroll
-        for (int t = 0; t < 8; ++t) {
-            float2 W = cmul(w1, K16p[t]);
-            float2 tb = cmul(W, v[t + 8]);
-            float2 a = v[t];
-            v[t] = cadd(a, tb);
-            v[t + 8] = csub(a, tb);
-        }
-    }
-
+    }
     float* orow = out + ((size_t)row << LOGN);
     #pragma unroll
-    for (int t = 0; t < 16; ++t)
-        orow[tid + (t << 9)] = v[t].x * (1.0f / (float)NN);
+    for (int t = 0; t < 8; ++t)
+        orow[tid + (t << 10)] = v[t].x * (1.0f / (float)NN);
 }
 
 extern "C" void kernel_launch(void* const* d_in, const int* in_sizes, int n_in,
@@ -854,8 +894,7 @@
     size_t need = (size_t)((char*)(fPg + NNODES) - ws);
     if (ws_size < need) return;
 
-    dim3 b(NT);
-    k_pre   <<<dim3(ROWS), b, 0, stream>>>(x, Lv16, Se, Coh, Ent, lfg, sig, hfg, cut);
-    k_decide<<<dim3(1),    b, 0, stream>>>(Se, Coh, Ent, fFg, fPg);
-    k_rest  <<<dim3(ROWS), b, 0, stream>>>(Lv16, Se, Coh, fFg, fPg, out, Wp, bp, Wo, bo, lfg, sig, hfg, cut);
-}
+    k_pre   <<<dim3(ROWS), dim3(NT),  0, stream>>>(x, Lv16, Se, Coh, Ent, lfg, sig, hfg, cut);
+    k_decide<<<dim3(1),    dim3(512), 0, stream>>>(Se, Coh, Ent, fFg, fPg);
+    k_rest  <<<dim3(ROWS), dim3(NT),  0, stream>>>(Lv16, Se, Coh, fFg, fPg, out, Wp, bp, Wo, bo, lfg, sig, hfg, cut);
+}
```

After: 174.7 us. 33.0% more time.
